# Optimization experiments

Measured on AMD Instinct MI355X. Metric: run time of the kernel, lower is better.

## Reference

```python
import jax, jax.numpy as jnp
import numpy as np

STRIDES = (8, 16, 32)
FMP = ((160, 160), (80, 80), (40, 40))
NUM_CLASSES = 80
TOPK = 1000
CONF_THRESH = 0.05
NMS_THRESH = 0.6
IMG_MAX = 1280.0
CLASS_OFFSET = 8192.0  # > any box coordinate, separates classes for batched NMS


def setup_inputs() -> dict:
    key = jax.random.key(0)
    ks = jax.random.split(key, 32)
    C = 256
    inp = {}
    for l, (h, w) in enumerate(FMP):
        inp[f'feat{l}'] = jax.random.normal(ks[l], (1, C, h, w), dtype=jnp.float32)
        inp[f'Wobj{l}'] = jax.random.normal(ks[3 + 6 * l + 0], (1, C), dtype=jnp.float32) * 0.05
        inp[f'bobj{l}'] = jnp.zeros((1,), dtype=jnp.float32)
        inp[f'Wcls{l}'] = jax.random.normal(ks[3 + 6 * l + 2], (NUM_CLASSES, C), dtype=jnp.float32) * 0.05
        inp[f'bcls{l}'] = jnp.zeros((NUM_CLASSES,), dtype=jnp.float32)
        inp[f'Wreg{l}'] = jax.random.normal(ks[3 + 6 * l + 4], (4, C), dtype=jnp.float32) * 0.05
        inp[f'breg{l}'] = jnp.zeros((4,), dtype=jnp.float32)
    return inp


def _level(feat, Wo, bo, Wc, bc, Wr, br, stride):
    x = feat[0]  # [C,H,W]
    H, W = x.shape[1], x.shape[2]
    def conv1x1(Wm, bv):
        # 1x1 conv == channel GEMM; output [H*W, O]
        return (jnp.einsum('oc,chw->hwo', Wm, x) + bv).reshape(H * W, -1)
    obj = conv1x1(Wo, bo)              # [M,1]
    cls = conv1x1(Wc, bc)              # [M,C]
    reg = jnp.exp(conv1x1(Wr, br)) * stride  # [M,4] (l,t,r,b)
    prob = jax.nn.sigmoid(obj) * jax.nn.sigmoid(cls)
    scores = prob.max(axis=-1)
    labels = prob.argmax(axis=-1)
    ay, ax = jnp.meshgrid(jnp.arange(H), jnp.arange(W), indexing='ij')
    anchors = (jnp.stack([ax, ay], axis=-1).astype(jnp.float32).reshape(-1, 2) + 0.5) * stride
    k = min(TOPK, H * W)
    scores, idx = jax.lax.top_k(scores, k)
    labels = labels[idx]
    reg = reg[idx]
    anchors = anchors[idx]
    boxes = jnp.concatenate([anchors - reg[:, :2], anchors + reg[:, 2:]], axis=-1)
    return scores, labels, boxes


def _batched_nms(boxes, scores, labels):
    N = boxes.shape[0]
    valid = scores >= CONF_THRESH
    # class-offset trick: per-class NMS == single NMS on disjoint offset boxes
    ob = boxes + labels.astype(boxes.dtype)[:, None] * CLASS_OFFSET
    order = jnp.argsort(-scores)
    b = ob[order]
    v = valid[order]
    x1, y1, x2, y2 = b[:, 0], b[:, 1], b[:, 2], b[:, 3]
    areas = (x2 - x1) * (y2 - y1)
    xx1 = jnp.maximum(x1[:, None], x1[None, :])
    yy1 = jnp.maximum(y1[:, None], y1[None, :])
    xx2 = jnp.minimum(x2[:, None], x2[None, :])
    yy2 = jnp.minimum(y2[:, None], y2[None, :])
    w = jnp.maximum(1e-10, xx2 - xx1)
    h = jnp.maximum(1e-10, yy2 - yy1)
    inter = w * h
    iou = inter / (areas[:, None] + areas[None, :] - inter + 1e-14)
    idxs = jnp.arange(N)
    def body(i, keep):
        sup = keep[i] & (iou[i] > NMS_THRESH) & (idxs > i)
        return keep & ~sup
    keep_sorted = jax.lax.fori_loop(0, N, body, v)
    keep = jnp.zeros(N, dtype=bool).at[order].set(keep_sorted)
    return keep


def reference(feat0, feat1, feat2,
              Wobj0, bobj0, Wcls0, bcls0, Wreg0, breg0,
              Wobj1, bobj1, Wcls1, bcls1, Wreg1, breg1,
              Wobj2, bobj2, Wcls2, bcls2, Wreg2, breg2):
    feats = (feat0, feat1, feat2)
    params = ((Wobj0, bobj0, Wcls0, bcls0, Wreg0, breg0),
              (Wobj1, bobj1, Wcls1, bcls1, Wreg1, breg1),
              (Wobj2, bobj2, Wcls2, bcls2, Wreg2, breg2))
    ss, ll, bb = [], [], []
    for l in range(3):
        s, lab, box = _level(feats[l], *params[l], STRIDES[l])
        ss.append(s); ll.append(lab); bb.append(box)
    scores = jnp.concatenate(ss)
    labels = jnp.concatenate(ll)
    boxes = jnp.concatenate(bb)
    keep = _batched_nms(boxes, scores, labels)
    bboxes = jnp.clip(boxes / IMG_MAX, 0.0, 1.0)
    return bboxes, scores, labels.astype(jnp.int32), keep
```

## Files before the change

kernel.cpp:

```cpp
#include <hip/hip_runtime.h>
#include <math.h>

#define NTOT   33600
#define NSEL   3000
#define CAND_CAP 8192
#define NWORDS 47
#define NROWS_PAD 3008
#define FCAP 4
#define NGRP 525
#define WPER 21760
#define NSLC 10
#define NTRI 1128

struct P21 {
  const float* feat[3];
  const float* Wobj[3];
  const float* bobj[3];
  const float* Wcls[3];
  const float* bcls[3];
  const float* Wreg[3];
  const float* breg[3];
};

__device__ __forceinline__ void level_of_group(int grp, int lane, int& l, int& p, int& g,
                                               int& HW, int& Wd, double& stride) {
  if (grp < 400)      { l = 0; p = grp * 64 + lane;         g = p;         HW = 25600; Wd = 160; stride = 8.0;  }
  else if (grp < 500) { l = 1; p = (grp - 400) * 64 + lane; g = 25600 + p; HW = 6400;  Wd = 80;  stride = 16.0; }
  else                { l = 2; p = (grp - 500) * 64 + lane; g = 32000 + p; HW = 1600;  Wd = 40;  stride = 32.0; }
}

__device__ __forceinline__ double sigmoid_d(double x) { return 1.0 / (1.0 + exp(-x)); }

__device__ __forceinline__ unsigned long long shfl64(unsigned long long v, int src) {
  unsigned lo = (unsigned)__shfl((int)(unsigned)(v & 0xFFFFFFFFull), src, 64);
  unsigned hi = (unsigned)__shfl((int)(unsigned)(v >> 32), src, 64);
  return (((unsigned long long)hi) << 32) | (unsigned long long)lo;
}

__global__ __launch_bounds__(256) void k_wconv(P21 P, double* __restrict__ W64) {
  int id = blockIdx.x * 256 + threadIdx.x;
  if (id >= 3 * WPER) return;
  int l = id / WPER, r = id - l * WPER;
  const float* src;
  if (r < 256)        src = P.Wobj[l] + r;
  else if (r < 1280)  src = P.Wreg[l] + (r - 256);
  else                src = P.Wcls[l] + (r - 1280);
  W64[id] = (double)(*src);
}

__global__ __launch_bounds__(128) void k_conv_chunk(P21 P, const double* __restrict__ W64,
    double* __restrict__ obj_t, double* __restrict__ reg_t,
    double* __restrict__ cmax, int* __restrict__ clab) {
  const int b = blockIdx.x, t = threadIdx.x;
  int l, p, g, HW;
  if (b < 100)      { l = 0; p = b * 256 + 2 * t;         g = p;         HW = 25600; }
  else if (b < 125) { l = 1; p = (b - 100) * 256 + 2 * t; g = 25600 + p; HW = 6400;  }
  else              { l = 2; p = (b - 125) * 256 + 2 * t; g = 32000 + p; HW = 1600;  }
  if (p >= HW) return;
  const int ch = blockIdx.y;
  const float* __restrict__ fp = P.feat[l] + p;
  const double* __restrict__ Wl = W64 + l * WPER;

  if (ch == 0) {
    const double* __restrict__ Wo = Wl;
    const double* __restrict__ Wr = Wl + 256;
    double o0 = (double)P.bobj[l][0], o1 = o0;
    double r0[4], r1[4];
#pragma unroll
    for (int j = 0; j < 4; j++) { r0[j] = (double)P.breg[l][j]; r1[j] = r0[j]; }
    for (int c = 0; c < 256; c += 8) {
      double x0[8], x1[8];
#pragma unroll
      for (int u = 0; u < 8; u++) {
        float2 v = *(const float2*)(fp + (c + u) * HW);
        x0[u] = (double)v.x; x1[u] = (double)v.y;
      }
#pragma unroll
      for (int u = 0; u < 8; u++) {
        double w = Wo[c + u];
        o0 = fma(w, x0[u], o0); o1 = fma(w, x1[u], o1);
#pragma unroll
        for (int j = 0; j < 4; j++) {
          double wr = Wr[j * 256 + c + u];
          r0[j] = fma(wr, x0[u], r0[j]); r1[j] = fma(wr, x1[u], r1[j]);
        }
      }
    }
    obj_t[g] = o0; obj_t[g + 1] = o1;
#pragma unroll
    for (int j = 0; j < 4; j++) { reg_t[4 * g + j] = r0[j]; reg_t[4 * g + 4 + j] = r1[j]; }
  } else {
    const int base = (ch - 1) * 8;
    const double* __restrict__ Wc = Wl + 1280 + base * 256;
    const float* __restrict__ bcls = P.bcls[l];
    double a0[8], a1[8];
#pragma unroll
    for (int j = 0; j < 8; j++) { a0[j] = (double)bcls[base + j]; a1[j] = a0[j]; }
    for (int c = 0; c < 256; c += 8) {
      double x0[8], x1[8];
#pragma unroll
      for (int u = 0; u < 8; u++) {
        float2 v = *(const float2*)(fp + (c + u) * HW);
        x0[u] = (double)v.x; x1[u] = (double)v.y;
      }
#pragma unroll
      for (int u = 0; u < 8; u++) {
#pragma unroll
        for (int j = 0; j < 8; j++) {
          double w = Wc[j * 256 + c + u];
          a0[j] = fma(w, x0[u], a0[j]); a1[j] = fma(w, x1[u], a1[j]);
        }
      }
    }
    double m0 = a0[0], m1 = a1[0]; int l0 = base, l1 = base;
#pragma unroll
    for (int j = 1; j < 8; j++) {
      if (a0[j] > m0) { m0 = a0[j]; l0 = base + j; }
      if (a1[j] > m1) { m1 = a1[j]; l1 = base + j; }
    }
    cmax[(ch - 1) * NTOT + g] = m0; cmax[(ch - 1) * NTOT + g + 1] = m1;
    clab[(ch - 1) * NTOT + g] = l0; clab[(ch - 1) * NTOT + g + 1] = l1;
  }
}

__global__ __launch_bounds__(64) void k_combine(
    const double* __restrict__ obj_t, const double* __restrict__ reg_t,
    const double* __restrict__ cmax, const int* __restrict__ clab,
    double* __restrict__ score_d, int* __restrict__ label_d,
    double* __restrict__ box_d, unsigned* __restrict__ hist) {
  int l, p, g, HW, Wd; double stride;
  level_of_group(blockIdx.x, threadIdx.x, l, p, g, HW, Wd, stride);

  double maxv = cmax[g]; int lab = clab[g];
#pragma unroll
  for (int k = 1; k < NSLC; k++) {
    double v = cmax[k * NTOT + g];
    int lb = clab[k * NTOT + g];
    if (v > maxv) { maxv = v; lab = lb; }
  }
  double score = sigmoid_d(obj_t[g]) * sigmoid_d(maxv);
  int h = p / Wd, w = p - h * Wd;
  double ax = ((double)w + 0.5) * stride;
  double ay = ((double)h + 0.5) * stride;
  double e0 = exp(reg_t[4 * g + 0]) * stride;
  double e1 = exp(reg_t[4 * g + 1]) * stride;
  double e2 = exp(reg_t[4 * g + 2]) * stride;
  double e3 = exp(reg_t[4 * g + 3]) * stride;

  score_d[g] = score;
  label_d[g] = lab;
  box_d[4 * g + 0] = ax - e0;
  box_d[4 * g + 1] = ay - e1;
  box_d[4 * g + 2] = ax + e2;
  box_d[4 * g + 3] = ay + e3;

  unsigned key = __float_as_uint((float)score);
  atomicAdd(&hist[l * 65536 + (key >> 16)], 1u);
}

__global__ __launch_bounds__(256) void k_scan_a(const unsigned* __restrict__ hist,
                                                unsigned* __restrict__ csG) {
  const int lane = threadIdx.x & 63;
  const int row = blockIdx.x * 4 + (threadIdx.x >> 6);
  const uint4* hp = (const uint4*)(hist + row * 256);
  uint4 v = hp[lane];
  unsigned s = v.x + v.y + v.z + v.w;
#pragma unroll
  for (int off = 32; off > 0; off >>= 1) s += (unsigned)__shfl_down((int)s, off, 64);
  if (lane == 0) csG[row] = s;
}

__global__ __launch_bounds__(256) void k_scan_b(const unsigned* __restrict__ hist,
                                                const unsigned* __restrict__ csG,
                                                unsigned* __restrict__ cutB) {
  int l = blockIdx.x;
  __shared__ unsigned cs[256];
  __shared__ unsigned hb[256];
  __shared__ int s_chunk;
  __shared__ unsigned s_acc;
  int t = threadIdx.x;
  cs[t] = csG[l * 256 + t];
  __syncthreads();
  if (t == 0) {
    unsigned acc = 0; int chunk = 0;
    for (int tt = 255; tt >= 0; tt--) {
      if (acc + cs[tt] >= 1000u) { chunk = tt; break; }
      acc += cs[tt];
    }
    s_chunk = chunk; s_acc = acc;
  }
  __syncthreads();
  int chunk = s_chunk;
  hb[t] = hist[l * 65536 + chunk * 256 + t];
  __syncthreads();
  if (t == 0) {
    unsigned acc = s_acc;
    unsigned B = (unsigned)(chunk * 256);
    for (int b = 255; b >= 0; b--) {
      unsigned c = hb[b];
      if (acc + c >= 1000u) { B = (unsigned)(chunk * 256 + b); break; }
      acc += c;
    }
    cutB[l] = B;
  }
}

__global__ __launch_bounds__(64) void k_compact(const double* __restrict__ score_d,
    const unsigned* __restrict__ cutB, unsigned* __restrict__ cnt,
    double* __restrict__ cand_s, int* __restrict__ cand_g) {
  int l, p, g, HW, Wd; double stride;
  level_of_group(blockIdx.x, threadIdx.x, l, p, g, HW, Wd, stride);
  double sc = score_d[g];
  unsigned key = __float_as_uint((float)sc);
  if ((key >> 16) >= cutB[l]) {
    unsigned pos = atomicAdd(&cnt[l], 1u);
    if (pos < CAND_CAP) {
      cand_s[l * CAND_CAP + pos] = sc;
      cand_g[l * CAND_CAP + pos] = g;
    }
  }
}

__global__ __launch_bounds__(256) void k_rank(const double* __restrict__ cand_s,
    const int* __restrict__ cand_g, const unsigned* __restrict__ cnt,
    const int* __restrict__ label_d, const double* __restrict__ box_d,
    double* __restrict__ sel_s, int* __restrict__ sel_lab, double* __restrict__ sel_box) {
  const int l = blockIdx.y;
  const int M = (int)min(cnt[l], (unsigned)CAND_CAP);
  if (blockIdx.x * 4 >= M) return;
  const int q = blockIdx.x * 4 + (threadIdx.x >> 6);
  const int lane = threadIdx.x & 63;
  const bool active = (q < M);

  double s = 0.0; int g = 0;
  if (active) { s = cand_s[l * CAND_CAP + q]; g = cand_g[l * CAND_CAP + q]; }

  int r = 0;
  if (active) {
    for (int j = lane; j < M; j += 64) {
      double sj = cand_s[l * CAND_CAP + j];
      int gj = cand_g[l * CAND_CAP + j];
      r += (sj > s) || (sj == s && gj < g);
    }
  }
#pragma unroll
  for (int off = 32; off > 0; off >>= 1) r += __shfl_down(r, off, 64);

  if (active && lane == 0 && r < 1000) {
    int o = l * 1000 + r;
    sel_s[o] = s;
    sel_lab[o] = label_d[g];
    sel_box[4 * o + 0] = box_d[4 * g + 0];
    sel_box[4 * o + 1] = box_d[4 * g + 1];
    sel_box[4 * o + 2] = box_d[4 * g + 2];
    sel_box[4 * o + 3] = box_d[4 * g + 3];
  }
}

__global__ __launch_bounds__(256) void k_order(const double* __restrict__ sel_s,
    const int* __restrict__ sel_lab, const double* __restrict__ sel_box,
    int* __restrict__ sortIdx, double* __restrict__ sbox, int* __restrict__ svalid) {
  const int i = blockIdx.x;
  const int t = threadIdx.x;
  const double s = sel_s[i];
  int r = 0;
  for (int j = t; j < NSEL; j += 256) {
    double sj = sel_s[j];
    r += (sj > s) || (sj == s && j < i);
  }
#pragma unroll
  for (int off = 32; off > 0; off >>= 1) r += __shfl_down(r, off, 64);
  __shared__ int wsum[4];
  if ((t & 63) == 0) wsum[t >> 6] = r;
  __syncthreads();
  if (t == 0) {
    int rr = wsum[0] + wsum[1] + wsum[2] + wsum[3];
    sortIdx[rr] = i;
    double off = (double)sel_lab[i] * 8192.0;
    sbox[4 * rr + 0] = sel_box[4 * i + 0] + off;
    sbox[4 * rr + 1] = sel_box[4 * i + 1] + off;
    sbox[4 * rr + 2] = sel_box[4 * i + 2] + off;
    sbox[4 * rr + 3] = sel_box[4 * i + 3] + off;
    svalid[rr] = (s >= 0.05) ? 1 : 0;
  }
}

__global__ __launch_bounds__(256) void k_mask(const double* __restrict__ sbox,
    unsigned long long* __restrict__ denseG, unsigned long long* __restrict__ diagG,
    unsigned short* __restrict__ entG, int* __restrict__ cntGi) {
  int k = blockIdx.x, rc = 0;
  while (k >= NWORDS - rc) { k -= NWORDS - rc; rc++; }
  const int w = rc + k;
  const int t = threadIdx.x, lane = t & 63, wk = t >> 6;
  const int rbase = rc * 64;
  __shared__ double rbox[256];
  {
    int idx = rbase * 4 + t;
    rbox[t] = (idx < NSEL * 4) ? sbox[idx] : 0.0;
  }
  const int j = w * 64 + lane;
  const bool jok = (j < NSEL);
  double bx1 = 0, by1 = 0, bx2 = 0, by2 = 0, arj = 0;
  if (jok) {
    bx1 = sbox[4 * j + 0]; by1 = sbox[4 * j + 1];
    bx2 = sbox[4 * j + 2]; by2 = sbox[4 * j + 3];
    arj = (bx2 - bx1) * (by2 - by1);
  }
  __syncthreads();
#pragma unroll
  for (int rr = 0; rr < 16; rr++) {
    const int ro = wk * 16 + rr;
    const int i = rbase + ro;
    if (i >= NSEL) break;
    double x1 = rbox[ro * 4 + 0], y1 = rbox[ro * 4 + 1];
    double x2 = rbox[ro * 4 + 2], y2 = rbox[ro * 4 + 3];
    double ar = (x2 - x1) * (y2 - y1);
    bool c = false;
    if (jok && j > i) {
      double xx1 = fmax(x1, bx1), yy1 = fmax(y1, by1);
      double xx2 = fmin(x2, bx2), yy2 = fmin(y2, by2);
      double ww = fmax(1e-10, xx2 - xx1);
      double hh = fmax(1e-10, yy2 - yy1);
      double inter = ww * hh;
      double iou = inter / (ar + arj - inter + 1e-14);
      c = iou > 0.6;
    }
    unsigned long long word = __ballot(c);
    if (lane == 0) {
      denseG[(size_t)i * 48 + w] = word;
      if (w == rc) diagG[i] = word;
      else if (word) {
        unsigned long long tt = word;
        while (tt) {
          int b = __builtin_ctzll(tt); tt &= tt - 1;
          int slot = atomicAdd(&cntGi[i], 1);
          if (slot < FCAP) entG[i * FCAP + slot] = (unsigned short)(w * 64 + b);
        }
      }
    }
  }
}

__global__ __launch_bounds__(256) void k_nms_scan(
    const unsigned long long* __restrict__ denseG, const unsigned long long* __restrict__ diagG,
    const unsigned short* __restrict__ entG, const int* __restrict__ cntGi,
    const int* __restrict__ svalid, const int* __restrict__ sortIdx,
    int* __restrict__ keepOrig) {
  __shared__ unsigned long long diagL[NROWS_PAD];
  __shared__ unsigned short entL[NROWS_PAD * FCAP];
  __shared__ unsigned short cntL[NROWS_PAD];
  __shared__ unsigned long long validL[48];
  __shared__ unsigned long long hasWL[48];
  const int t = threadIdx.x;
  const int lane = t & 63;

  for (int k = t; k < NSEL; k += 256) diagL[k] = diagG[k];
  for (int k = NSEL + t; k < NROWS_PAD; k += 256) diagL[k] = 0ull;
  uint2* e2 = (uint2*)entL; const uint2* eg2 = (const uint2*)entG;
  for (int k = t; k < NSEL; k += 256) e2[k] = eg2[k];
  for (int k = NSEL + t; k < NROWS_PAD; k += 256) { uint2 z; z.x = 0; z.y = 0; e2[k] = z; }
  for (int k = t; k < NSEL; k += 256) cntL[k] = (unsigned short)cntGi[k];
  for (int k = NSEL + t; k < NROWS_PAD; k += 256) cntL[k] = 0;
  for (int i0 = t; i0 < NROWS_PAD; i0 += 256) {
    bool f = (i0 < NSEL) && (svalid[i0] != 0);
    unsigned long long b = __ballot(f);
    if ((t & 63) == 0) validL[i0 >> 6] = b;
  }
  __syncthreads();
  if (t >= 64) return;

  for (int w = 0; w < NWORDS; w++) {
    int i = w * 64 + lane;
    bool f = (diagL[i] != 0ull) || (cntL[i] != 0);
    unsigned long long b = __ballot(f);
    if (lane == 0) hasWL[w] = b;
  }

  unsigned long long rem = 0ull;
  unsigned long long keep = 0ull;
  for (int w = 0; w < NWORDS; w++) {
    unsigned long long vw = validL[w];
    unsigned long long remw = shfl64(rem, w);
    unsigned long long win = vw & ~remw;
    unsigned long long work = hasWL[w];
    while (work) {
      int d = __builtin_ctzll(work); work &= work - 1;
      if ((win >> d) & 1ull) {
        int i = w * 64 + d;
        win &= ~diagL[i];
        int c = cntL[i];
        if (c > FCAP) {
          unsigned long long rowj = (lane < NWORDS) ? denseG[(size_t)i * 48 + lane] : 0ull;
          rem |= rowj;
        } else {
          for (int k = 0; k < c; k++) {
            int j = entL[i * FCAP + k];
            if ((j >> 6) == lane) rem |= 1ull << (j & 63);
          }
        }
      }
    }
    if (lane == w) keep = win;
  }
  if (lane < NWORDS) {
    for (int b = 0; b < 64; b++) {
      int j = lane * 64 + b;
      if (j < NSEL) keepOrig[sortIdx[j]] = (int)((keep >> b) & 1ull);
    }
  }
}

__global__ __launch_bounds__(256) void k_out(const double* __restrict__ sel_s,
    const int* __restrict__ sel_lab, const double* __restrict__ sel_box,
    const int* __restrict__ keepOrig, float* __restrict__ out) {
  int i = blockIdx.x * 256 + threadIdx.x;
  if (i >= NSEL) return;
#pragma unroll
  for (int c = 0; c < 4; c++) {
    double v = sel_box[4 * i + c] / 1280.0;
    v = fmin(fmax(v, 0.0), 1.0);
    out[4 * i + c] = (float)v;
  }
  out[12000 + i] = (float)sel_s[i];
  out[15000 + i] = (float)sel_lab[i];
  out[18000 + i] = keepOrig[i] ? 1.0f : 0.0f;
}

extern "C" void kernel_launch(void* const* d_in, const int* in_sizes, int n_in,
                              void* d_out, int out_size, void* d_ws, size_t ws_size,
                              hipStream_t stream) {
  P21 P;
  for (int l = 0; l < 3; l++) {
    P.feat[l] = (const float*)d_in[7 * l + 0];
    P.Wobj[l] = (const float*)d_in[7 * l + 1];
    P.bobj[l] = (const float*)d_in[7 * l + 2];
    P.Wcls[l] = (const float*)d_in[7 * l + 3];
    P.bcls[l] = (const float*)d_in[7 * l + 4];
    P.Wreg[l] = (const float*)d_in[7 * l + 5];
    P.breg[l] = (const float*)d_in[7 * l + 6];
  }

  char* ws = (char*)d_ws;
  size_t off = 0;
  auto alloc = [&](size_t bytes) -> char* {
    char* p = ws + off;
    off += (bytes + 15) & ~(size_t)15;
    return p;
  };
  double* score_d  = (double*)alloc((size_t)NTOT * 8);
  double* box_d    = (double*)alloc((size_t)NTOT * 4 * 8);
  int*    label_d  = (int*)   alloc((size_t)NTOT * 4);
  double* obj_t    = (double*)alloc((size_t)NTOT * 8);
  double* reg_t    = (double*)alloc((size_t)NTOT * 4 * 8);
  double* cmax     = (double*)alloc((size_t)NSLC * NTOT * 8);
  int*    clab     = (int*)   alloc((size_t)NSLC * NTOT * 4);
  double* W64      = (double*)alloc((size_t)3 * WPER * 8);
  double* sel_s    = (double*)alloc((size_t)NSEL * 8);
  double* sel_box  = (double*)alloc((size_t)NSEL * 4 * 8);
  int*    sel_lab  = (int*)   alloc((size_t)NSEL * 4);
  int*    sortIdx  = (int*)   alloc((size_t)NSEL * 4);
  double* sbox     = (double*)alloc((size_t)NSEL * 4 * 8);
  int*    svalid   = (int*)   alloc((size_t)NSEL * 4);
  int*    keepOrig = (int*)   alloc((size_t)NSEL * 4);
  double* cand_s   = (double*)alloc((size_t)3 * CAND_CAP * 8);
  int*    cand_g   = (int*)   alloc((size_t)3 * CAND_CAP * 4);
  unsigned long long* denseG = (unsigned long long*)alloc((size_t)NSEL * 48 * 8);
  unsigned long long* diagG  = (unsigned long long*)alloc((size_t)NSEL * 8);
  unsigned short*     entG   = (unsigned short*)alloc((size_t)NSEL * FCAP * 2);
  unsigned* hist   = (unsigned*)alloc((size_t)3 * 65536 * 4);
  unsigned* cnt    = (unsigned*)alloc(16);
  int*      cntGi  = (int*)   alloc((size_t)NSEL * 4);
  unsigned* cutB   = (unsigned*)alloc(16);
  unsigned* csG    = (unsigned*)alloc((size_t)768 * 4);

  hipMemsetAsync(hist, 0, (size_t)3 * 65536 * 4 + 16 + (size_t)NSEL * 4, stream);
  hipMemsetAsync(denseG, 0, (size_t)NSEL * 48 * 8, stream);

  k_wconv   <<<(3 * WPER + 255) / 256, 256, 0, stream>>>(P, W64);
  dim3 cgrid(132, 11, 1);
  k_conv_chunk<<<cgrid, 128, 0, stream>>>(P, W64, obj_t, reg_t, cmax, clab);
  k_combine <<<NGRP, 64, 0, stream>>>(obj_t, reg_t, cmax, clab, score_d, label_d, box_d, hist);
  k_scan_a  <<<192, 256, 0, stream>>>(hist, csG);
  k_scan_b  <<<3, 256, 0, stream>>>(hist, csG, cutB);
  k_compact <<<NGRP, 64, 0, stream>>>(score_d, cutB, cnt, cand_s, cand_g);
  dim3 rgrid(CAND_CAP / 4, 3, 1);
  k_rank    <<<rgrid, 256, 0, stream>>>(cand_s, cand_g, cnt, label_d, box_d,
                                        sel_s, sel_lab, sel_box);
  k_order   <<<NSEL, 256, 0, stream>>>(sel_s, sel_lab, sel_box, sortIdx, sbox, svalid);
  k_mask    <<<NTRI, 256, 0, stream>>>(sbox, denseG, diagG, entG, cntGi);
  k_nms_scan<<<1, 256, 0, stream>>>(denseG, diagG, entG, cntGi, svalid, sortIdx, keepOrig);
  k_out     <<<(NSEL + 255) / 256, 256, 0, stream>>>(sel_s, sel_lab, sel_box, keepOrig, (float*)d_out);
}
```

Before: 277.6 us.

## Fuse small kernels and memsets, prefetch conv channel loads

The two memsets and the weight conversion are folded into one setup kernel that zeroes the histogram and counters. The two-stage histogram scan becomes a single kernel, and the NMS scan is merged with output writing, so the keep flags stay in shared memory instead of a global buffer. The FP64 1x1-conv kernel moves to 256-thread blocks over flattened pixel pairs and register double-buffers the next 8 channel loads to hide memory latency. The aim is fewer launches and less exposed latency. The risks are that the denseG memset is dropped, which relies on k_mask writing every row that is later read, and that the single-block scan kernel is more serial.

```diff
diff --git a/kernel.cpp b/kernel.cpp
--- a/kernel.cpp
+++ b/kernel.cpp
@@ -11,6 +11,8 @@
 #define WPER 21760
 #define NSLC 10
 #define NTRI 1128
+#define NPAIR 16800
+#define ZTOT 199612
 
 struct P21 {
   const float* feat[3];
@@ -37,29 +39,38 @@
   return (((unsigned long long)hi) << 32) | (unsigned long long)lo;
 }
 
-__global__ __launch_bounds__(256) void k_wconv(P21 P, double* __restrict__ W64) {
+__global__ __launch_bounds__(256) void k_setup(P21 P, unsigned* __restrict__ zbase,
+                                               double* __restrict__ W64) {
   int id = blockIdx.x * 256 + threadIdx.x;
-  if (id >= 3 * WPER) return;
-  int l = id / WPER, r = id - l * WPER;
-  const float* src;
-  if (r < 256)        src = P.Wobj[l] + r;
-  else if (r < 1280)  src = P.Wreg[l] + (r - 256);
-  else                src = P.Wcls[l] + (r - 1280);
-  W64[id] = (double)(*src);
-}
-
-__global__ __launch_bounds__(128) void k_conv_chunk(P21 P, const double* __restrict__ W64,
+  if (id < ZTOT) zbase[id] = 0;
+  if (id < 3 * WPER) {
+    int l = id / WPER, r = id - l * WPER;
+    const float* src;
+    if (r < 256)        src = P.Wobj[l] + r;
+    else if (r < 1280)  src = P.Wreg[l] + (r - 256);
+    else                src = P.Wcls[l] + (r - 1280);
+    W64[id] = (double)(*src);
+  }
+}
+
+__global__ __launch_bounds__(256) void k_conv_chunk(P21 P, const double* __restrict__ W64,
     double* __restrict__ obj_t, double* __restrict__ reg_t,
     double* __restrict__ cmax, int* __restrict__ clab) {
-  const int b = blockIdx.x, t = threadIdx.x;
-  int l, p, g, HW;
-  if (b < 100)      { l = 0; p = b * 256 + 2 * t;         g = p;         HW = 25600; }
-  else if (b < 125) { l = 1; p = (b - 100) * 256 + 2 * t; g = 25600 + p; HW = 6400;  }
-  else              { l = 2; p = (b - 125) * 256 + 2 * t; g = 32000 + p; HW = 1600;  }
-  if (p >= HW) return;
+  const int q = blockIdx.x * 256 + threadIdx.x;
+  if (q >= NPAIR) return;
+  int l, p, g;
+  if (q < 12800)      { l = 0; p = 2 * q;             g = p; }
+  else if (q < 16000) { l = 1; p = 2 * (q - 12800);   g = 25600 + p; }
+  else                { l = 2; p = 2 * (q - 16000);   g = 32000 + p; }
+  const int HW = (l == 0) ? 25600 : (l == 1) ? 6400 : 1600;
+  const int s2 = HW >> 1;
   const int ch = blockIdx.y;
-  const float* __restrict__ fp = P.feat[l] + p;
+  const float2* __restrict__ fp2 = (const float2*)(P.feat[l] + p);
   const double* __restrict__ Wl = W64 + l * WPER;
+
+  float2 cur[8], nxt[8];
+#pragma unroll
+  for (int u = 0; u < 8; u++) cur[u] = fp2[u * s2];
 
   if (ch == 0) {
     const double* __restrict__ Wo = Wl;
@@ -69,22 +80,22 @@
 #pragma unroll
     for (int j = 0; j < 4; j++) { r0[j] = (double)P.breg[l][j]; r1[j] = r0[j]; }
     for (int c = 0; c < 256; c += 8) {
-      double x0[8], x1[8];
+      const int cn = (c + 8 < 256) ? (c + 8) : 248;
+#pragma unroll
+      for (int u = 0; u < 8; u++) nxt[u] = fp2[(cn + u) * s2];
 #pragma unroll
       for (int u = 0; u < 8; u++) {
-        float2 v = *(const float2*)(fp + (c + u) * HW);
-        x0[u] = (double)v.x; x1[u] = (double)v.y;
-      }
-#pragma unroll
-      for (int u = 0; u < 8; u++) {
+        double x0 = (double)cur[u].x, x1 = (double)cur[u].y;
         double w = Wo[c + u];
-        o0 = fma(w, x0[u], o0); o1 = fma(w, x1[u], o1);
+        o0 = fma(w, x0, o0); o1 = fma(w, x1, o1);
 #pragma unroll
         for (int j = 0; j < 4; j++) {
           double wr = Wr[j * 256 + c + u];
-          r0[j] = fma(wr, x0[u], r0[j]); r1[j] = fma(wr, x1[u], r1[j]);
+          r0[j] = fma(wr, x0, r0[j]); r1[j] = fma(wr, x1, r1[j]);
         }
       }
+#pragma unroll
+      for (int u = 0; u < 8; u++) cur[u] = nxt[u];
     }
     obj_t[g] = o0; obj_t[g + 1] = o1;
 #pragma unroll
@@ -97,20 +108,20 @@
 #pragma unroll
     for (int j = 0; j < 8; j++) { a0[j] = (double)bcls[base + j]; a1[j] = a0[j]; }
     for (int c = 0; c < 256; c += 8) {
-      double x0[8], x1[8];
+      const int cn = (c + 8 < 256) ? (c + 8) : 248;
+#pragma unroll
+      for (int u = 0; u < 8; u++) nxt[u] = fp2[(cn + u) * s2];
 #pragma unroll
       for (int u = 0; u < 8; u++) {
-        float2 v = *(const float2*)(fp + (c + u) * HW);
-        x0[u] = (double)v.x; x1[u] = (double)v.y;
-      }
-#pragma unroll
-      for (int u = 0; u < 8; u++) {
+        double x0 = (double)cur[u].x, x1 = (double)cur[u].y;
 #pragma unroll
         for (int j = 0; j < 8; j++) {
           double w = Wc[j * 256 + c + u];
-          a0[j] = fma(w, x0[u], a0[j]); a1[j] = fma(w, x1[u], a1[j]);
+          a0[j] = fma(w, x0, a0[j]); a1[j] = fma(w, x1, a1[j]);
         }
       }
+#pragma unroll
+      for (int u = 0; u < 8; u++) cur[u] = nxt[u];
     }
     double m0 = a0[0], m1 = a1[0]; int l0 = base, l1 = base;
 #pragma unroll
@@ -158,28 +169,21 @@
   atomicAdd(&hist[l * 65536 + (key >> 16)], 1u);
 }
 
-__global__ __launch_bounds__(256) void k_scan_a(const unsigned* __restrict__ hist,
-                                                unsigned* __restrict__ csG) {
-  const int lane = threadIdx.x & 63;
-  const int row = blockIdx.x * 4 + (threadIdx.x >> 6);
-  const uint4* hp = (const uint4*)(hist + row * 256);
-  uint4 v = hp[lane];
-  unsigned s = v.x + v.y + v.z + v.w;
-#pragma unroll
-  for (int off = 32; off > 0; off >>= 1) s += (unsigned)__shfl_down((int)s, off, 64);
-  if (lane == 0) csG[row] = s;
-}
-
-__global__ __launch_bounds__(256) void k_scan_b(const unsigned* __restrict__ hist,
-                                                const unsigned* __restrict__ csG,
-                                                unsigned* __restrict__ cutB) {
+__global__ __launch_bounds__(256) void k_scan(const unsigned* __restrict__ hist,
+                                              unsigned* __restrict__ cutB) {
   int l = blockIdx.x;
+  const unsigned* h = hist + l * 65536;
   __shared__ unsigned cs[256];
   __shared__ unsigned hb[256];
   __shared__ int s_chunk;
   __shared__ unsigned s_acc;
   int t = threadIdx.x;
-  cs[t] = csG[l * 256 + t];
+  {
+    const uint4* hp = (const uint4*)(h + t * 256);
+    unsigned s = 0;
+    for (int b = 0; b < 64; b++) { uint4 v = hp[b]; s += v.x + v.y + v.z + v.w; }
+    cs[t] = s;
+  }
   __syncthreads();
   if (t == 0) {
     unsigned acc = 0; int chunk = 0;
@@ -191,7 +195,7 @@
   }
   __syncthreads();
   int chunk = s_chunk;
-  hb[t] = hist[l * 65536 + chunk * 256 + t];
+  hb[t] = h[chunk * 256 + t];
   __syncthreads();
   if (t == 0) {
     unsigned acc = s_acc;
@@ -341,16 +345,19 @@
   }
 }
 
-__global__ __launch_bounds__(256) void k_nms_scan(
+__global__ __launch_bounds__(256) void k_final(
     const unsigned long long* __restrict__ denseG, const unsigned long long* __restrict__ diagG,
     const unsigned short* __restrict__ entG, const int* __restrict__ cntGi,
     const int* __restrict__ svalid, const int* __restrict__ sortIdx,
-    int* __restrict__ keepOrig) {
+    const double* __restrict__ sel_s, const int* __restrict__ sel_lab,
+    const double* __restrict__ sel_box, float* __restrict__ out) {
   __shared__ unsigned long long diagL[NROWS_PAD];
   __shared__ unsigned short entL[NROWS_PAD * FCAP];
   __shared__ unsigned short cntL[NROWS_PAD];
   __shared__ unsigned long long validL[48];
   __shared__ unsigned long long hasWL[48];
+  __shared__ unsigned long long keepWL[48];
+  __shared__ unsigned char keepO[NROWS_PAD];
   const int t = threadIdx.x;
   const int lane = t & 63;
 
@@ -367,63 +374,58 @@
     if ((t & 63) == 0) validL[i0 >> 6] = b;
   }
   __syncthreads();
-  if (t >= 64) return;
-
-  for (int w = 0; w < NWORDS; w++) {
-    int i = w * 64 + lane;
-    bool f = (diagL[i] != 0ull) || (cntL[i] != 0);
-    unsigned long long b = __ballot(f);
-    if (lane == 0) hasWL[w] = b;
-  }
-
-  unsigned long long rem = 0ull;
-  unsigned long long keep = 0ull;
-  for (int w = 0; w < NWORDS; w++) {
-    unsigned long long vw = validL[w];
-    unsigned long long remw = shfl64(rem, w);
-    unsigned long long win = vw & ~remw;
-    unsigned long long work = hasWL[w];
-    while (work) {
-      int d = __builtin_ctzll(work); work &= work - 1;
-      if ((win >> d) & 1ull) {
-        int i = w * 64 + d;
-        win &= ~diagL[i];
-        int c = cntL[i];
-        if (c > FCAP) {
-          unsigned long long rowj = (lane < NWORDS) ? denseG[(size_t)i * 48 + lane] : 0ull;
-          rem |= rowj;
-        } else {
-          for (int k = 0; k < c; k++) {
-            int j = entL[i * FCAP + k];
-            if ((j >> 6) == lane) rem |= 1ull << (j & 63);
+
+  if (t < 64) {
+    for (int w = 0; w < NWORDS; w++) {
+      int i = w * 64 + lane;
+      bool f = (diagL[i] != 0ull) || (cntL[i] != 0);
+      unsigned long long b = __ballot(f);
+      if (lane == 0) hasWL[w] = b;
+    }
+    unsigned long long rem = 0ull;
+    unsigned long long keep = 0ull;
+    for (int w = 0; w < NWORDS; w++) {
+      unsigned long long vw = validL[w];
+      unsigned long long remw = shfl64(rem, w);
+      unsigned long long win = vw & ~remw;
+      unsigned long long work = hasWL[w];
+      while (work) {
+        int d = __builtin_ctzll(work); work &= work - 1;
+        if ((win >> d) & 1ull) {
+          int i = w * 64 + d;
+          win &= ~diagL[i];
+          int c = cntL[i];
+          if (c > FCAP) {
+            unsigned long long rowj = (lane < NWORDS) ? denseG[(size_t)i * 48 + lane] : 0ull;
+            rem |= rowj;
+          } else {
+            for (int k = 0; k < c; k++) {
+              int j = entL[i * FCAP + k];
+              if ((j >> 6) == lane) rem |= 1ull << (j & 63);
+            }
           }
         }
       }
-    }
-    if (lane == w) keep = win;
-  }
-  if (lane < NWORDS) {
-    for (int b = 0; b < 64; b++) {
-      int j = lane * 64 + b;
-      if (j < NSEL) keepOrig[sortIdx[j]] = (int)((keep >> b) & 1ull);
-    }
-  }
-}
-
-__global__ __launch_bounds__(256) void k_out(const double* __restrict__ sel_s,
-    const int* __restrict__ sel_lab, const double* __restrict__ sel_box,
-    const int* __restrict__ keepOrig, float* __restrict__ out) {
-  int i = blockIdx.x * 256 + threadIdx.x;
-  if (i >= NSEL) return;
-#pragma unroll
-  for (int c = 0; c < 4; c++) {
-    double v = sel_box[4 * i + c] / 1280.0;
-    v = fmin(fmax(v, 0.0), 1.0);
-    out[4 * i + c] = (float)v;
-  }
-  out[12000 + i] = (float)sel_s[i];
-  out[15000 + i] = (float)sel_lab[i];
-  out[18000 + i] = keepOrig[i] ? 1.0f : 0.0f;
+      if (lane == w) keep = win;
+    }
+    if (lane < NWORDS) keepWL[lane] = keep;
+  }
+  __syncthreads();
+
+  for (int r = t; r < NSEL; r += 256)
+    keepO[sortIdx[r]] = (unsigned char)((keepWL[r >> 6] >> (r & 63)) & 1ull);
+  __syncthreads();
+  for (int i = t; i < NSEL; i += 256) {
+#pragma unroll
+    for (int c = 0; c < 4; c++) {
+      double v = sel_box[4 * i + c] / 1280.0;
+      v = fmin(fmax(v, 0.0), 1.0);
+      out[4 * i + c] = (float)v;
+    }
+    out[12000 + i] = (float)sel_s[i];
+    out[15000 + i] = (float)sel_lab[i];
+    out[18000 + i] = keepO[i] ? 1.0f : 0.0f;
+  }
 }
 
 extern "C" void kernel_launch(void* const* d_in, const int* in_sizes, int n_in,
@@ -461,7 +463,6 @@
   int*    sortIdx  = (int*)   alloc((size_t)NSEL * 4);
   double* sbox     = (double*)alloc((size_t)NSEL * 4 * 8);
   int*    svalid   = (int*)   alloc((size_t)NSEL * 4);
-  int*    keepOrig = (int*)   alloc((size_t)NSEL * 4);
   double* cand_s   = (double*)alloc((size_t)3 * CAND_CAP * 8);
   int*    cand_g   = (int*)   alloc((size_t)3 * CAND_CAP * 4);
   unsigned long long* denseG = (unsigned long long*)alloc((size_t)NSEL * 48 * 8);
@@ -471,23 +472,18 @@
   unsigned* cnt    = (unsigned*)alloc(16);
   int*      cntGi  = (int*)   alloc((size_t)NSEL * 4);
   unsigned* cutB   = (unsigned*)alloc(16);
-  unsigned* csG    = (unsigned*)alloc((size_t)768 * 4);
-
-  hipMemsetAsync(hist, 0, (size_t)3 * 65536 * 4 + 16 + (size_t)NSEL * 4, stream);
-  hipMemsetAsync(denseG, 0, (size_t)NSEL * 48 * 8, stream);
-
-  k_wconv   <<<(3 * WPER + 255) / 256, 256, 0, stream>>>(P, W64);
-  dim3 cgrid(132, 11, 1);
-  k_conv_chunk<<<cgrid, 128, 0, stream>>>(P, W64, obj_t, reg_t, cmax, clab);
+
+  k_setup   <<<(ZTOT + 255) / 256, 256, 0, stream>>>(P, hist, W64);
+  dim3 cgrid(66, 11, 1);
+  k_conv_chunk<<<cgrid, 256, 0, stream>>>(P, W64, obj_t, reg_t, cmax, clab);
   k_combine <<<NGRP, 64, 0, stream>>>(obj_t, reg_t, cmax, clab, score_d, label_d, box_d, hist);
-  k_scan_a  <<<192, 256, 0, stream>>>(hist, csG);
-  k_scan_b  <<<3, 256, 0, stream>>>(hist, csG, cutB);
+  k_scan    <<<3, 256, 0, stream>>>(hist, cutB);
   k_compact <<<NGRP, 64, 0, stream>>>(score_d, cutB, cnt, cand_s, cand_g);
   dim3 rgrid(CAND_CAP / 4, 3, 1);
   k_rank    <<<rgrid, 256, 0, stream>>>(cand_s, cand_g, cnt, label_d, box_d,
                                         sel_s, sel_lab, sel_box);
   k_order   <<<NSEL, 256, 0, stream>>>(sel_s, sel_lab, sel_box, sortIdx, sbox, svalid);
   k_mask    <<<NTRI, 256, 0, stream>>>(sbox, denseG, diagG, entG, cntGi);
-  k_nms_scan<<<1, 256, 0, stream>>>(denseG, diagG, entG, cntGi, svalid, sortIdx, keepOrig);
-  k_out     <<<(NSEL + 255) / 256, 256, 0, stream>>>(sel_s, sel_lab, sel_box, keepOrig, (float*)d_out);
-}
+  k_final   <<<1, 256, 0, stream>>>(denseG, diagG, entG, cntGi, svalid, sortIdx,
+                                    sel_s, sel_lab, sel_box, (float*)d_out);
+}
```

Measured after the change: 339.0 us. 1.22x slower.
